# Kernel optimization log

Hardware: AMD Instinct MI355X
Metric: run time of the kernel (lower is better)

Reference implementation:

```python
import jax, jax.numpy as jnp
import numpy as np

B, S, HID = 2, 2048, 1024
H, D = 16, 64  # num query heads, head_dim; single shared KV head
SCALE = D ** -0.5


def setup_inputs() -> dict:
    key = jax.random.key(0)
    k1, k2, k3, k4, k5 = jax.random.split(key, 5)
    return {
        "hidden_states": jax.random.normal(k1, (B, S, HID), dtype=jnp.float32),
        "Wq": jax.random.normal(k2, (HID, HID), dtype=jnp.float32) * 0.02,
        "Wk": jax.random.normal(k3, (HID, D), dtype=jnp.float32) * 0.02,
        "Wv": jax.random.normal(k4, (HID, D), dtype=jnp.float32) * 0.02,
        "Wo": jax.random.normal(k5, (HID, HID), dtype=jnp.float32) * 0.02,
    }


def reference(hidden_states, Wq, Wk, Wv, Wo):
    b, s, _ = hidden_states.shape
    # projections: Q has H heads; K/V have a single shared head of dim D
    q = (hidden_states @ Wq).reshape(b, s, H, D)  # [B,S,H,D]
    k = hidden_states @ Wk                        # [B,S,D]
    v = hidden_states @ Wv                        # [B,S,D]
    # scores: broadcast single KV head across all query heads
    scores = jnp.einsum("bqhd,bkd->bhqk", q, k) * SCALE  # [B,H,S,S]
    attn = jax.nn.softmax(scores, axis=-1)
    out = jnp.einsum("bhqk,bkd->bqhd", attn, v).reshape(b, s, HID)
    return out @ Wo
```

## Files before the change

### kernel.cpp

```cpp
#include <hip/hip_runtime.h>
#include <math.h>

#define BATCH 2
#define SEQ   2048
#define HID   1024
#define NH    16
#define HD    64
#define MTOT  (BATCH * SEQ)

#define PST 72
#define VST 136
#define WTS 69

#define EXP_C1 0.1803368801111255f

typedef __attribute__((ext_vector_type(8))) short short8;
typedef __attribute__((ext_vector_type(4))) float floatx4;
typedef __attribute__((ext_vector_type(16))) float floatx16;
typedef __attribute__((ext_vector_type(4))) unsigned int uint4v;

#define MFMA32(a, b, c) __builtin_amdgcn_mfma_f32_32x32x16_bf16(a, b, c, 0, 0, 0)
#define MFMA16(a, b, c) __builtin_amdgcn_mfma_f32_16x16x32_bf16(a, b, c, 0, 0, 0)

static __device__ __forceinline__ floatx16 zero16() {
    floatx16 z;
    #pragma unroll
    for (int i = 0; i < 16; ++i) z[i] = 0.f;
    return z;
}

__device__ __forceinline__ unsigned short f2bf(float x) {
    unsigned u = __float_as_uint(x);
    u += 0x7FFF + ((u >> 16) & 1);
    return (unsigned short)(u >> 16);
}
__device__ __forceinline__ float bf2f(unsigned short h) {
    return __uint_as_float((unsigned)h << 16);
}
__device__ __forceinline__ void split16(const float* f, unsigned short* hh, unsigned short* ll) {
    #pragma unroll
    for (int e = 0; e < 16; ++e) {
        unsigned short h = f2bf(f[e]);
        hh[e] = h;
        ll[e] = f2bf(f[e] - bf2f(h));
    }
}

__device__ __forceinline__ void gld16(const unsigned short* g, unsigned short* l) {
    __builtin_amdgcn_global_load_lds(
        (const __attribute__((address_space(1))) unsigned int*)g,
        (__attribute__((address_space(3))) unsigned int*)l, 16, 0, 0);
}


__global__ __launch_bounds__(256)
void presplit_kernel(const float* __restrict__ Wq, const float* __restrict__ Wk,
                     const float* __restrict__ Wv, const float* __restrict__ Wo,
                     const float* __restrict__ X,
                     unsigned short* __restrict__ WqTh, unsigned short* __restrict__ WqTl,
                     unsigned short* __restrict__ WkTh, unsigned short* __restrict__ WkTl,
                     unsigned short* __restrict__ WvTh, unsigned short* __restrict__ WvTl,
                     unsigned short* __restrict__ WoTh, unsigned short* __restrict__ WoTl,
                     unsigned short* __restrict__ Xh)
{
    __shared__ __align__(16) float Wtmp[64][WTS];
    const int tid = threadIdx.x;
    int bx = blockIdx.x;

    if (bx >= 544) {
        size_t i0 = (size_t)(bx - 544) * 4096 + tid * 16;
        float f[16];
        *(float4*)&f[0]  = *(const float4*)(X + i0 + 0);
        *(float4*)&f[4]  = *(const float4*)(X + i0 + 4);
        *(float4*)&f[8]  = *(const float4*)(X + i0 + 8);
        *(float4*)&f[12] = *(const float4*)(X + i0 + 12);
        unsigned short hh[16];
        #pragma unroll
        for (int e = 0; e < 16; ++e) hh[e] = f2bf(f[e]);
        const int m  = (bx - 544) * 4 + (tid >> 6);
        const int k0 = (tid & 63) * 16;
        const int m32 = m >> 5, mi = (m >> 4) & 1, tr = m & 15;
        #pragma unroll
        for (int c = 0; c < 2; ++c) {
            const int k = k0 + c * 8;
            const int ktx = k >> 6, ksx = (k >> 5) & 1, qd = (k >> 3) & 3;
            size_t off = (((size_t)(m32 * 16 + ktx) * 2 + ksx) * 2 + mi) * 512
                       + (qd * 16 + tr) * 8;
            *(uint4*)(Xh + off) = *(uint4*)&hh[c * 8];
        }
        return;
    }

    const float* W; unsigned short *Th, *Tl; int ldw, kt, nt;
    if (bx < 256)      { W = Wq; Th = WqTh; Tl = WqTl; ldw = HID; kt = bx >> 4; nt = bx & 15; }
    else if (bx < 272) { W = Wk; Th = WkTh; Tl = WkTl; ldw = HD;  kt = bx - 256; nt = 0; }
    else if (bx < 288) { W = Wv; Th = WvTh; Tl = WvTl; ldw = HD;  kt = bx - 272; nt = 0; }
    else               { W = Wo; Th = WoTh; Tl = WoTl; ldw = HID; bx -= 288; kt = bx >> 4; nt = bx & 15; }
    const int k0 = kt * 64, n0 = nt * 64;

    {
        const int wk = tid >> 2, wn = (tid & 3) * 16;
        const float* wp = W + (size_t)(k0 + wk) * ldw + n0 + wn;
        float f[16];
        *(float4*)&f[0]  = *(const float4*)(wp + 0);
        *(float4*)&f[4]  = *(const float4*)(wp + 4);
        *(float4*)&f[8]  = *(const float4*)(wp + 8);
        *(float4*)&f[12] = *(const float4*)(wp + 12);
        #pragma unroll
        for (int e = 0; e < 16; ++e) Wtmp[wk][wn + e] = f[e];
    }
    __syncthreads();
    {
        const int rn = tid >> 2, rk = (tid & 3) * 16;
        float f[16];
        #pragma unroll
        for (int e = 0; e < 16; ++e) f[e] = Wtmp[rk + e][rn];
        unsigned short hh[16], ll[16];
        split16(f, hh, ll);
        const int sub = rn >> 4, tw = rn & 15;
        const size_t tb = ((size_t)nt * 16 + kt) * 4096;
        const int ksA = rk >> 5,       qA = (rk >> 3) & 3;
        const int ksB = (rk + 8) >> 5, qB = ((rk + 8) >> 3) & 3;
        const size_t offA = tb + (size_t)(ksA * 4 + sub) * 512 + (qA * 16 + tw) * 8;
        const size_t offB = tb + (size_t)(ksB * 4 + sub) * 512 + (qB * 16 + tw) * 8;
        *(uint4*)(Th + offA) = *(uint4*)&hh[0];
        *(uint4*)(Th + offB) = *(uint4*)&hh[8];
        *(uint4*)(Tl + offA) = *(uint4*)&ll[0];
        *(uint4*)(Tl + offB) = *(uint4*)&ll[8];
    }
}

__global__ __launch_bounds__(256)
void qkv_kernel(const unsigned short* __restrict__ Xfo,
                const unsigned short* __restrict__ WqTh, const unsigned short* __restrict__ WqTl,
                const unsigned short* __restrict__ WkTh, const unsigned short* __restrict__ WkTl,
                const unsigned short* __restrict__ WvTh, const unsigned short* __restrict__ WvTl,
                unsigned short* __restrict__ Qh,
                unsigned short* __restrict__ Kh, unsigned short* __restrict__ Vth)
{
    __shared__ __align__(16) unsigned short Wst[2][2][4096];

    const int tid  = threadIdx.x;
    const int wave = tid >> 6, lane = tid & 63;
    const int t = lane & 15, quad = lane >> 4;
    const int m0 = blockIdx.x * 128;
    const int nb = blockIdx.y;

    const unsigned short *WTh, *WTl; int nt;
    if (nb < 16)       { WTh = WqTh; WTl = WqTl; nt = nb; }
    else if (nb == 16) { WTh = WkTh; WTl = WkTl; nt = 0; }
    else               { WTh = WvTh; WTl = WvTl; nt = 0; }

    floatx4 acc[2][4];
    #pragma unroll
    for (int mi = 0; mi < 2; ++mi)
        #pragma unroll
        for (int sub = 0; sub < 4; ++sub) acc[mi][sub] = (floatx4){0.f,0.f,0.f,0.f};

    const size_t abase = ((size_t)(blockIdx.x * 4 + wave) * 16) * 2048 + lane * 8;
    const int g0 = wave * 2;

    auto STAGE = [&](int buf, int kt) {
        const size_t tb = ((size_t)nt * 16 + kt) * 4096 + g0 * 512 + lane * 8;
        gld16(WTh + tb,       &Wst[buf][0][g0 * 512]);
        gld16(WTh + tb + 512, &Wst[buf][0][g0 * 512 + 512]);
        gld16(WTl + tb,       &Wst[buf][1][g0 * 512]);
        gld16(WTl + tb + 512, &Wst[buf][1][g0 * 512 + 512]);
    };
    auto COMPUTE = [&](int buf, short8 a00, short8 a01, short8 a10, short8 a11) {
        #pragma unroll
        for (int ksq = 0; ksq < 2; ++ksq) {
            short8 am0 = ksq ? a10 : a00;
            short8 am1 = ksq ? a11 : a01;
            #pragma unroll
            for (int sub = 0; sub < 4; ++sub) {
                const int g = ksq * 4 + sub;
                short8 bh = *(const short8*)&Wst[buf][0][g * 512 + lane * 8];
                short8 bl = *(const short8*)&Wst[buf][1][g * 512 + lane * 8];
                acc[0][sub] = MFMA16(am0, bh, acc[0][sub]);
                acc[0][sub] = MFMA16(am0, bl, acc[0][sub]);
                acc[1][sub] = MFMA16(am1, bh, acc[1][sub]);
                acc[1][sub] = MFMA16(am1, bl, acc[1][sub]);
            }
        }
    };

    short8 a00, a01, a10, a11;
    {
        const unsigned short* ab = Xfo + abase;
        a00 = *(const short8*)(ab);
        a01 = *(const short8*)(ab + 512);
        a10 = *(const short8*)(ab + 1024);
        a11 = *(const short8*)(ab + 1536);
    }
    STAGE(0, 0);
    __syncthreads();

    int cur = 0;
    for (int kt = 0; kt < HID / 64 - 1; ++kt) {
        STAGE(cur ^ 1, kt + 1);
        const unsigned short* ab = Xfo + abase + (size_t)(kt + 1) * 2048;
        short8 n00 = *(const short8*)(ab);
        short8 n01 = *(const short8*)(ab + 512);
        short8 n10 = *(const short8*)(ab + 1024);
        short8 n11 = *(const short8*)(ab + 1536);

        COMPUTE(cur, a00, a01, a10, a11);

        __syncthreads();
        a00 = n00; a01 = n01; a10 = n10; a11 = n11;
        cur ^= 1;
    }
    COMPUTE(cur, a00, a01, a10, a11);

    #pragma unroll
    for (int mi = 0; mi < 2; ++mi)
        #pragma unroll
        for (int sub = 0; sub < 4; ++sub)
            #pragma unroll
            for (int r = 0; r < 4; ++r) {
                int g = m0 + wave * 32 + mi * 16 + quad * 4 + r;
                int d = sub * 16 + t;
                if (nb < 16) {
                    int b = g >> 11, s = g & (SEQ - 1);
                    Qh[((size_t)(b * NH + nb) * SEQ + s) * HD + d] =
                        f2bf(acc[mi][sub][r] * EXP_C1);
                } else if (nb == 16) {
                    Kh[(size_t)g * HD + d] = f2bf(acc[mi][sub][r]);
                } else {
                    int b = g >> 11, s = g & (SEQ - 1);
                    Vth[(size_t)b * HD * SEQ + (size_t)d * SEQ + s] = f2bf(acc[mi][sub][r]);
                }
            }
}

__global__ __launch_bounds__(512, 4)
void flash_kernel(const unsigned short* __restrict__ Qhg,
                  const unsigned short* __restrict__ Khg,
                  const unsigned short* __restrict__ Vthg,
                  unsigned short* __restrict__ Oh)
{
    __shared__ __align__(16) char smem[35840];
    unsigned short (*Ksh)[PST] = (unsigned short (*)[PST])smem;
    unsigned short (*Vsh)[VST] = (unsigned short (*)[VST])(smem + 18432);

    const int tid  = threadIdx.x;
    const int wave = tid >> 6, lane = tid & 63;
    const int lq = lane & 31, hi = lane >> 5;
    const int qw = wave >> 1;
    const int ks = wave & 1;
    const int klq = (lq & ~12) | ((lq & 4) << 1) | ((lq & 8) >> 1);

    const int q0 = blockIdx.x * 128;
    const int h  = blockIdx.y;
    const int b  = blockIdx.z;

    short8 qreg[4];
    {
        const unsigned short* qp =
            Qhg + ((size_t)(b * NH + h) * SEQ + q0 + qw * 32 + lq) * HD + hi * 8;
        #pragma unroll
        for (int dc = 0; dc < 4; ++dc) qreg[dc] = *(const short8*)(qp + dc * 16);
    }

    const unsigned short* Kh_b  = Khg  + (size_t)b * SEQ * HD;
    const unsigned short* Vth_b = Vthg + (size_t)b * HD * SEQ;

    const int krA = tid >> 3,          kcA = (tid & 7) * 8;
    const int krB = 64 + (tid >> 3),   kcB = kcA;
    const int vrA = tid >> 4,          vcA = (tid & 15) * 8;
    const int vrB = 32 + (tid >> 4),   vcB = vcA;

    floatx16 o0 = zero16(), o1 = zero16(), ol = zero16();
    short8 onesB;
    #pragma unroll
    for (int j = 0; j < 8; ++j) onesB[j] = (short)0x3F80;

    uint4 gk0 = *(const uint4*)(Kh_b + (size_t)krA * HD + kcA);
    uint4 gk1 = *(const uint4*)(Kh_b + (size_t)krB * HD + kcB);
    uint4 gv0 = *(const uint4*)(Vth_b + (size_t)vrA * SEQ + vcA);
    uint4 gv1 = *(const uint4*)(Vth_b + (size_t)vrB * SEQ + vcB);

    for (int kt = 0; kt < SEQ / 128; ++kt) {
        __syncthreads();
        *(uint4*)&Ksh[krA][kcA] = gk0;
        *(uint4*)&Ksh[krB][kcB] = gk1;
        *(uint4*)&Vsh[vrA][vcA] = gv0;
        *(uint4*)&Vsh[vrB][vcB] = gv1;
        if (kt + 1 < SEQ / 128) {
            gk0 = *(const uint4*)(Kh_b + (size_t)((kt + 1) * 128 + krA) * HD + kcA);
            gk1 = *(const uint4*)(Kh_b + (size_t)((kt + 1) * 128 + krB) * HD + kcB);
            gv0 = *(const uint4*)(Vth_b + (size_t)vrA * SEQ + (kt + 1) * 128 + vcA);
            gv1 = *(const uint4*)(Vth_b + (size_t)vrB * SEQ + (kt + 1) * 128 + vcB);
        }
        __syncthreads();

        #pragma unroll
        for (int c = 0; c < 2; ++c) {
            const int kb = ks * 64 + c * 32;

            floatx16 sf = zero16();
            __builtin_amdgcn_s_setprio(1);
            #pragma unroll
            for (int dc = 0; dc < 4; ++dc) {
                short8 kf = *(const short8*)&Ksh[kb + klq][dc * 16 + hi * 8];
                sf = MFMA32(kf, qreg[dc], sf);
            }
            __builtin_amdgcn_s_setprio(0);

            #pragma unroll
            for (int mm = 0; mm < 2; ++mm) {
                unsigned uu[8];
                #pragma unroll
                for (int j = 0; j < 8; ++j)
                    uu[j] = __float_as_uint(exp2f(sf[mm * 8 + j]));
                uint4v pw;
                pw.x = (uu[0] >> 16) | (uu[1] & 0xFFFF0000u);
                pw.y = (uu[2] >> 16) | (uu[3] & 0xFFFF0000u);
                pw.z = (uu[4] >> 16) | (uu[5] & 0xFFFF0000u);
                pw.w = (uu[6] >> 16) | (uu[7] & 0xFFFF0000u);
                short8 pa = __builtin_bit_cast(short8, pw);
                short8 v0 = *(const short8*)&Vsh[lq][kb + mm * 16 + hi * 8];
                short8 v1 = *(const short8*)&Vsh[32 + lq][kb + mm * 16 + hi * 8];
                __builtin_amdgcn_s_setprio(1);
                ol = MFMA32(pa, onesB, ol);
                o0 = MFMA32(pa, v0, o0);
                o1 = MFMA32(pa, v1, o1);
                __builtin_amdgcn_s_setprio(0);
            }
        }
    }

    __syncthreads();
    float* cb  = (float*)smem;
    float* cbl = (float*)(smem + 33792);
    const int cbase = (qw * 64 + lane) * 33;
    if (ks) {
        #pragma unroll
        for (int r = 0; r < 16; ++r) { cb[cbase + r] = o0[r]; cb[cbase + 16 + r] = o1[r]; }
        if (lq == 0) {
            #pragma unroll
            for (int r = 0; r < 16; ++r) cbl[(qw * 2 + hi) * 16 + r] = ol[r];
        }
    }
    __syncthreads();
    if (!ks) {
        const int m32 = b * 64 + blockIdx.x * 4 + qw;
        #pragma unroll
        for (int r = 0; r < 16; ++r) {
            int qr = (r & 3) + 8 * (r >> 2) + 4 * hi;
            float ltot = ol[r] + cbl[(qw * 2 + hi) * 16 + r];
            float inv = 1.0f / ltot;
            float a0 = o0[r] + cb[cbase + r];
            float a1 = o1[r] + cb[cbase + 16 + r];
            int mi = qr >> 4, tr = qr & 15;
            size_t base = (((size_t)(m32 * 16 + h) * 2 + 0) * 2 + mi) * 512
                        + ((lq >> 3) * 16 + tr) * 8 + (lq & 7);
            Oh[base]        = f2bf(a0 * inv);
            Oh[base + 1024] = f2bf(a1 * inv);
        }
    }
}

__global__ __launch_bounds__(256)
void out_proj_kernel(const unsigned short* __restrict__ Ofo,
                     const unsigned short* __restrict__ WoTh,
                     const unsigned short* __restrict__ WoTl,
                     float* __restrict__ out)
{
    __shared__ __align__(16) unsigned short Wst[2][2][4096];

    const int tid  = threadIdx.x;
    const int wave = tid >> 6, lane = tid & 63;
    const int t = lane & 15, quad = lane >> 4;
    const int m0 = blockIdx.x * 128;
    const int nt = blockIdx.y;

    floatx4 acc[2][4];
    #pragma unroll
    for (int mi = 0; mi < 2; ++mi)
        #pragma unroll
        for (int sub = 0; sub < 4; ++sub) acc[mi][sub] = (floatx4){0.f,0.f,0.f,0.f};

    const size_t abase = ((size_t)(blockIdx.x * 4 + wave) * 16) * 2048 + lane * 8;
    const int g0 = wave * 2;

    auto STAGE = [&](int buf, int kt) {
        const size_t tb = ((size_t)nt * 16 + kt) * 4096 + g0 * 512 + lane * 8;
        gld16(WoTh + tb,       &Wst[buf][0][g0 * 512]);
        gld16(WoTh + tb + 512, &Wst[buf][0][g0 * 512 + 512]);
        gld16(WoTl + tb,       &Wst[buf][1][g0 * 512]);
        gld16(WoTl + tb + 512, &Wst[buf][1][g0 * 512 + 512]);
    };
    auto COMPUTE = [&](int buf, short8 a00, short8 a01, short8 a10, short8 a11) {
        #pragma unroll
        for (int ksq = 0; ksq < 2; ++ksq) {
            short8 am0 = ksq ? a10 : a00;
            short8 am1 = ksq ? a11 : a01;
            #pragma unroll
            for (int sub = 0; sub < 4; ++sub) {
                const int g = ksq * 4 + sub;
                short8 bh = *(const short8*)&Wst[buf][0][g * 512 + lane * 8];
                short8 bl = *(const short8*)&Wst[buf][1][g * 512 + lane * 8];
                acc[0][sub] = MFMA16(am0, bh, acc[0][sub]);
                acc[0][sub] = MFMA16(am0, bl, acc[0][sub]);
                acc[1][sub] = MFMA16(am1, bh, acc[1][sub]);
                acc[1][sub] = MFMA16(am1, bl, acc[1][sub]);
            }
        }
    };

    short8 a00, a01, a10, a11;
    {
        const unsigned short* ab = Ofo + abase;
        a00 = *(const short8*)(ab);
        a01 = *(const short8*)(ab + 512);
        a10 = *(const short8*)(ab + 1024);
        a11 = *(const short8*)(ab + 1536);
    }
    STAGE(0, 0);
    __syncthreads();

    int cur = 0;
    for (int kt = 0; kt < HID / 64 - 1; ++kt) {
        STAGE(cur ^ 1, kt + 1);
        const unsigned short* ab = Ofo + abase + (size_t)(kt + 1) * 2048;
        short8 n00 = *(const short8*)(ab);
        short8 n01 = *(const short8*)(ab + 512);
        short8 n10 = *(const short8*)(ab + 1024);
        short8 n11 = *(const short8*)(ab + 1536);

        COMPUTE(cur, a00, a01, a10, a11);

        __syncthreads();
        a00 = n00; a01 = n01; a10 = n10; a11 = n11;
        cur ^= 1;
    }
    COMPUTE(cur, a00, a01, a10, a11);

    const int n0 = nt * 64;
    #pragma unroll
    for (int mi = 0; mi < 2; ++mi)
        #pragma unroll
        for (int sub = 0; sub < 4; ++sub)
            #pragma unroll
            for (int r = 0; r < 4; ++r)
                out[(size_t)(m0 + wave * 32 + mi * 16 + quad * 4 + r) * HID
                    + n0 + sub * 16 + t] = acc[mi][sub][r];
}

extern "C" void kernel_launch(void* const* d_in, const int* in_sizes, int n_in,
                              void* d_out, int out_size, void* d_ws, size_t ws_size,
                              hipStream_t stream)
{
    const float* X  = (const float*)d_in[0];
    const float* Wq = (const float*)d_in[1];
    const float* Wk = (const float*)d_in[2];
    const float* Wv = (const float*)d_in[3];
    const float* Wo = (const float*)d_in[4];
    float* out = (float*)d_out;

    unsigned short* Qh = (unsigned short*)d_out;
    unsigned short* Xh = Qh + (size_t)BATCH * NH * SEQ * HD;

    char* ws = (char*)d_ws;
    const size_t SZ_WQ = (size_t)HID * HID * 2;
    const size_t SZ_WK = (size_t)HD * HID * 2;
    unsigned short* WqTh = (unsigned short*)(ws);
    unsigned short* WqTl = (unsigned short*)(ws + SZ_WQ);
    unsigned short* WkTh = (unsigned short*)(ws + 2*SZ_WQ);
    unsigned short* WkTl = (unsigned short*)(ws + 2*SZ_WQ + SZ_WK);
    unsigned short* WvTh = (unsigned short*)(ws + 2*SZ_WQ + 2*SZ_WK);
    unsigned short* WvTl = (unsigned short*)(ws + 2*SZ_WQ + 3*SZ_WK);
    unsigned short* WoTh = (unsigned short*)(ws + 2*SZ_WQ + 4*SZ_WK);
    unsigned short* WoTl = (unsigned short*)(ws + 3*SZ_WQ + 4*SZ_WK);
    unsigned short* Kh   = (unsigned short*)(ws + 4*SZ_WQ + 4*SZ_WK);
    unsigned short* Vth  = (unsigned short*)(ws + 4*SZ_WQ + 4*SZ_WK + (size_t)MTOT*HD*2);
    unsigned short* Oh   = (unsigned short*)(ws + 4*SZ_WQ + 4*SZ_WK + (size_t)MTOT*HD*4);

    presplit_kernel<<<dim3(1568), 256, 0, stream>>>(Wq, Wk, Wv, Wo, X,
        WqTh, WqTl, WkTh, WkTl, WvTh, WvTl, WoTh, WoTl, Xh);
    qkv_kernel<<<dim3(MTOT / 128, 18), 256, 0, stream>>>(Xh,
        WqTh, WqTl, WkTh, WkTl, WvTh, WvTl, Qh, Kh, Vth);
    flash_kernel<<<dim3(SEQ / 128, NH, BATCH), 512, 0, stream>>>(Qh, Kh, Vth, Oh);
    out_proj_kernel<<<dim3(MTOT / 128, HID / 64), 256, 0, stream>>>(Oh, WoTh, WoTl, out);
}
```

Baseline: 174.4 us.

## Drop low-half weight split in QKV projection and widen GEMM blocks to 512 threads

```diff
diff --git a/kernel.cpp b/kernel.cpp
--- a/kernel.cpp
+++ b/kernel.cpp
@@ -37,14 +37,6 @@
 __device__ __forceinline__ float bf2f(unsigned short h) {
     return __uint_as_float((unsigned)h << 16);
 }
-__device__ __forceinline__ void split16(const float* f, unsigned short* hh, unsigned short* ll) {
-    #pragma unroll
-    for (int e = 0; e < 16; ++e) {
-        unsigned short h = f2bf(f[e]);
-        hh[e] = h;
-        ll[e] = f2bf(f[e] - bf2f(h));
-    }
-}
 
 __device__ __forceinline__ void gld16(const unsigned short* g, unsigned short* l) {
     __builtin_amdgcn_global_load_lds(
@@ -57,9 +49,9 @@
 void presplit_kernel(const float* __restrict__ Wq, const float* __restrict__ Wk,
                      const float* __restrict__ Wv, const float* __restrict__ Wo,
                      const float* __restrict__ X,
-                     unsigned short* __restrict__ WqTh, unsigned short* __restrict__ WqTl,
-                     unsigned short* __restrict__ WkTh, unsigned short* __restrict__ WkTl,
-                     unsigned short* __restrict__ WvTh, unsigned short* __restrict__ WvTl,
+                     unsigned short* __restrict__ WqTh,
+                     unsigned short* __restrict__ WkTh,
+                     unsigned short* __restrict__ WvTh,
                      unsigned short* __restrict__ WoTh, unsigned short* __restrict__ WoTl,
                      unsigned short* __restrict__ Xh)
 {
@@ -92,10 +84,10 @@
     }
 
     const float* W; unsigned short *Th, *Tl; int ldw, kt, nt;
-    if (bx < 256)      { W = Wq; Th = WqTh; Tl = WqTl; ldw = HID; kt = bx >> 4; nt = bx & 15; }
-    else if (bx < 272) { W = Wk; Th = WkTh; Tl = WkTl; ldw = HD;  kt = bx - 256; nt = 0; }
-    else if (bx < 288) { W = Wv; Th = WvTh; Tl = WvTl; ldw = HD;  kt = bx - 272; nt = 0; }
-    else               { W = Wo; Th = WoTh; Tl = WoTl; ldw = HID; bx -= 288; kt = bx >> 4; nt = bx & 15; }
+    if (bx < 256)      { W = Wq; Th = WqTh; Tl = nullptr; ldw = HID; kt = bx >> 4; nt = bx & 15; }
+    else if (bx < 272) { W = Wk; Th = WkTh; Tl = nullptr; ldw = HD;  kt = bx - 256; nt = 0; }
+    else if (bx < 288) { W = Wv; Th = WvTh; Tl = nullptr; ldw = HD;  kt = bx - 272; nt = 0; }
+    else               { W = Wo; Th = WoTh; Tl = WoTl;   ldw = HID; bx -= 288; kt = bx >> 4; nt = bx & 15; }
     const int k0 = kt * 64, n0 = nt * 64;
 
     {
@@ -115,8 +107,9 @@
         float f[16];
         #pragma unroll
         for (int e = 0; e < 16; ++e) f[e] = Wtmp[rk + e][rn];
-        unsigned short hh[16], ll[16];
-        split16(f, hh, ll);
+        unsigned short hh[16];
+        #pragma unroll
+        for (int e = 0; e < 16; ++e) hh[e] = f2bf(f[e]);
         const int sub = rn >> 4, tw = rn & 15;
         const size_t tb = ((size_t)nt * 16 + kt) * 4096;
         const int ksA = rk >> 5,       qA = (rk >> 3) & 3;
@@ -125,20 +118,25 @@
         const size_t offB = tb + (size_t)(ksB * 4 + sub) * 512 + (qB * 16 + tw) * 8;
         *(uint4*)(Th + offA) = *(uint4*)&hh[0];
         *(uint4*)(Th + offB) = *(uint4*)&hh[8];
-        *(uint4*)(Tl + offA) = *(uint4*)&ll[0];
-        *(uint4*)(Tl + offB) = *(uint4*)&ll[8];
-    }
-}
-
-__global__ __launch_bounds__(256)
+        if (Tl) {
+            unsigned short ll[16];
+            #pragma unroll
+            for (int e = 0; e < 16; ++e) ll[e] = f2bf(f[e] - bf2f(hh[e]));
+            *(uint4*)(Tl + offA) = *(uint4*)&ll[0];
+            *(uint4*)(Tl + offB) = *(uint4*)&ll[8];
+        }
+    }
+}
+
+__global__ __launch_bounds__(512)
 void qkv_kernel(const unsigned short* __restrict__ Xfo,
-                const unsigned short* __restrict__ WqTh, const unsigned short* __restrict__ WqTl,
-                const unsigned short* __restrict__ WkTh, const unsigned short* __restrict__ WkTl,
-                const unsigned short* __restrict__ WvTh, const unsigned short* __restrict__ WvTl,
+                const unsigned short* __restrict__ WqTh,
+                const unsigned short* __restrict__ WkTh,
+                const unsigned short* __restrict__ WvTh,
                 unsigned short* __restrict__ Qh,
                 unsigned short* __restrict__ Kh, unsigned short* __restrict__ Vth)
 {
-    __shared__ __align__(16) unsigned short Wst[2][2][4096];
+    __shared__ __align__(16) unsigned short Wst[2][4096];
 
     const int tid  = threadIdx.x;
     const int wave = tid >> 6, lane = tid & 63;
@@ -146,92 +144,70 @@
     const int m0 = blockIdx.x * 128;
     const int nb = blockIdx.y;
 
-    const unsigned short *WTh, *WTl; int nt;
-    if (nb < 16)       { WTh = WqTh; WTl = WqTl; nt = nb; }
-    else if (nb == 16) { WTh = WkTh; WTl = WkTl; nt = 0; }
-    else               { WTh = WvTh; WTl = WvTl; nt = 0; }
-
-    floatx4 acc[2][4];
-    #pragma unroll
-    for (int mi = 0; mi < 2; ++mi)
-        #pragma unroll
-        for (int sub = 0; sub < 4; ++sub) acc[mi][sub] = (floatx4){0.f,0.f,0.f,0.f};
-
-    const size_t abase = ((size_t)(blockIdx.x * 4 + wave) * 16) * 2048 + lane * 8;
-    const int g0 = wave * 2;
+    const unsigned short *WTh; int nt;
+    if (nb < 16)       { WTh = WqTh; nt = nb; }
+    else if (nb == 16) { WTh = WkTh; nt = 0; }
+    else               { WTh = WvTh; nt = 0; }
+
+    floatx4 acc[4];
+    #pragma unroll
+    for (int sub = 0; sub < 4; ++sub) acc[sub] = (floatx4){0.f,0.f,0.f,0.f};
+
+    const int m32 = blockIdx.x * 4 + (wave >> 1), mi = wave & 1;
+    const size_t abase = ((size_t)m32 * 16) * 2048 + (size_t)mi * 512 + lane * 8;
 
     auto STAGE = [&](int buf, int kt) {
-        const size_t tb = ((size_t)nt * 16 + kt) * 4096 + g0 * 512 + lane * 8;
-        gld16(WTh + tb,       &Wst[buf][0][g0 * 512]);
-        gld16(WTh + tb + 512, &Wst[buf][0][g0 * 512 + 512]);
-        gld16(WTl + tb,       &Wst[buf][1][g0 * 512]);
-        gld16(WTl + tb + 512, &Wst[buf][1][g0 * 512 + 512]);
+        const size_t tb = ((size_t)nt * 16 + kt) * 4096 + wave * 512 + lane * 8;
+        gld16(WTh + tb, &Wst[buf][wave * 512]);
     };
-    auto COMPUTE = [&](int buf, short8 a00, short8 a01, short8 a10, short8 a11) {
+    auto COMPUTE = [&](int buf, short8 a0, short8 a1) {
         #pragma unroll
         for (int ksq = 0; ksq < 2; ++ksq) {
-            short8 am0 = ksq ? a10 : a00;
-            short8 am1 = ksq ? a11 : a01;
+            short8 am = ksq ? a1 : a0;
             #pragma unroll
             for (int sub = 0; sub < 4; ++sub) {
-                const int g = ksq * 4 + sub;
-                short8 bh = *(const short8*)&Wst[buf][0][g * 512 + lane * 8];
-                short8 bl = *(const short8*)&Wst[buf][1][g * 512 + lane * 8];
-                acc[0][sub] = MFMA16(am0, bh, acc[0][sub]);
-                acc[0][sub] = MFMA16(am0, bl, acc[0][sub]);
-                acc[1][sub] = MFMA16(am1, bh, acc[1][sub]);
-                acc[1][sub] = MFMA16(am1, bl, acc[1][sub]);
+                short8 bh = *(const short8*)&Wst[buf][(ksq * 4 + sub) * 512 + lane * 8];
+                acc[sub] = MFMA16(am, bh, acc[sub]);
             }
         }
     };
 
-    short8 a00, a01, a10, a11;
-    {
-        const unsigned short* ab = Xfo + abase;
-        a00 = *(const short8*)(ab);
-        a01 = *(const short8*)(ab + 512);
-        a10 = *(const short8*)(ab + 1024);
-        a11 = *(const short8*)(ab + 1536);
-    }
+    short8 a0 = *(const short8*)(Xfo + abase);
+    short8 a1 = *(const short8*)(Xfo + abase + 1024);
     STAGE(0, 0);
     __syncthreads();
 
     int cur = 0;
     for (int kt = 0; kt < HID / 64 - 1; ++kt) {
         STAGE(cur ^ 1, kt + 1);
-        const unsigned short* ab = Xfo + abase + (size_t)(kt + 1) * 2048;
-        short8 n00 = *(const short8*)(ab);
-        short8 n01 = *(const short8*)(ab + 512);
-        short8 n10 = *(const short8*)(ab + 1024);
-        short8 n11 = *(const short8*)(ab + 1536);
-
-        COMPUTE(cur, a00, a01, a10, a11);
+        short8 n0 = *(const short8*)(Xfo + abase + (size_t)(kt + 1) * 2048);
+        short8 n1 = *(const short8*)(Xfo + abase + (size_t)(kt + 1) * 2048 + 1024);
+
+        COMPUTE(cur, a0, a1);
 
         __syncthreads();
-        a00 = n00; a01 = n01; a10 = n10; a11 = n11;
+        a0 = n0; a1 = n1;
         cur ^= 1;
     }
-    COMPUTE(cur, a00, a01, a10, a11);
-
-    #pragma unroll
-    for (int mi = 0; mi < 2; ++mi)
-        #pragma unroll
-        for (int sub = 0; sub < 4; ++sub)
-            #pragma unroll
-            for (int r = 0; r < 4; ++r) {
-                int g = m0 + wave * 32 + mi * 16 + quad * 4 + r;
-                int d = sub * 16 + t;
-                if (nb < 16) {
-                    int b = g >> 11, s = g & (SEQ - 1);
-                    Qh[((size_t)(b * NH + nb) * SEQ + s) * HD + d] =
-                        f2bf(acc[mi][sub][r] * EXP_C1);
-                } else if (nb == 16) {
-                    Kh[(size_t)g * HD + d] = f2bf(acc[mi][sub][r]);
-                } else {
-                    int b = g >> 11, s = g & (SEQ - 1);
-                    Vth[(size_t)b * HD * SEQ + (size_t)d * SEQ + s] = f2bf(acc[mi][sub][r]);
-                }
+    COMPUTE(cur, a0, a1);
+
+    #pragma unroll
+    for (int sub = 0; sub < 4; ++sub)
+        #pragma unroll
+        for (int r = 0; r < 4; ++r) {
+            int g = m0 + wave * 16 + quad * 4 + r;
+            int d = sub * 16 + t;
+            if (nb < 16) {
+                int b = g >> 11, s = g & (SEQ - 1);
+                Qh[((size_t)(b * NH + nb) * SEQ + s) * HD + d] =
+                    f2bf(acc[sub][r] * EXP_C1);
+            } else if (nb == 16) {
+                Kh[(size_t)g * HD + d] = f2bf(acc[sub][r]);
+            } else {
+                int b = g >> 11, s = g & (SEQ - 1);
+                Vth[(size_t)b * HD * SEQ + (size_t)d * SEQ + s] = f2bf(acc[sub][r]);
             }
+        }
 }
 
 __global__ __launch_bounds__(512, 4)
@@ -362,7 +338,7 @@
     }
 }
 
-__global__ __launch_bounds__(256)
+__global__ __launch_bounds__(512)
 void out_proj_kernel(const unsigned short* __restrict__ Ofo,
                      const unsigned short* __restrict__ WoTh,
                      const unsigned short* __restrict__ WoTl,
@@ -376,77 +352,58 @@
     const int m0 = blockIdx.x * 128;
     const int nt = blockIdx.y;
 
-    floatx4 acc[2][4];
-    #pragma unroll
-    for (int mi = 0; mi < 2; ++mi)
-        #pragma unroll
-        for (int sub = 0; sub < 4; ++sub) acc[mi][sub] = (floatx4){0.f,0.f,0.f,0.f};
-
-    const size_t abase = ((size_t)(blockIdx.x * 4 + wave) * 16) * 2048 + lane * 8;
-    const int g0 = wave * 2;
+    floatx4 acc[4];
+    #pragma unroll
+    for (int sub = 0; sub < 4; ++sub) acc[sub] = (floatx4){0.f,0.f,0.f,0.f};
+
+    const int m32 = blockIdx.x * 4 + (wave >> 1), mi = wave & 1;
+    const size_t abase = ((size_t)m32 * 16) * 2048 + (size_t)mi * 512 + lane * 8;
 
     auto STAGE = [&](int buf, int kt) {
-        const size_t tb = ((size_t)nt * 16 + kt) * 4096 + g0 * 512 + lane * 8;
-        gld16(WoTh + tb,       &Wst[buf][0][g0 * 512]);
-        gld16(WoTh + tb + 512, &Wst[buf][0][g0 * 512 + 512]);
-        gld16(WoTl + tb,       &Wst[buf][1][g0 * 512]);
-        gld16(WoTl + tb + 512, &Wst[buf][1][g0 * 512 + 512]);
+        const size_t tb = ((size_t)nt * 16 + kt) * 4096 + wave * 512 + lane * 8;
+        gld16(WoTh + tb, &Wst[buf][0][wave * 512]);
+        gld16(WoTl + tb, &Wst[buf][1][wave * 512]);
     };
-    auto COMPUTE = [&](int buf, short8 a00, short8 a01, short8 a10, short8 a11) {
+    auto COMPUTE = [&](int buf, short8 a0, short8 a1) {
         #pragma unroll
         for (int ksq = 0; ksq < 2; ++ksq) {
-            short8 am0 = ksq ? a10 : a00;
-            short8 am1 = ksq ? a11 : a01;
+            short8 am = ksq ? a1 : a0;
             #pragma unroll
             for (int sub = 0; sub < 4; ++sub) {
-                const int g = ksq * 4 + sub;
-                short8 bh = *(const short8*)&Wst[buf][0][g * 512 + lane * 8];
-                short8 bl = *(const short8*)&Wst[buf][1][g * 512 + lane * 8];
-                acc[0][sub] = MFMA16(am0, bh, acc[0][sub]);
-                acc[0][sub] = MFMA16(am0, bl, acc[0][sub]);
-                acc[1][sub] = MFMA16(am1, bh, acc[1][sub]);
-                acc[1][sub] = MFMA16(am1, bl, acc[1][sub]);
+                short8 bh = *(const short8*)&Wst[buf][0][(ksq * 4 + sub) * 512 + lane * 8];
+                short8 bl = *(const short8*)&Wst[buf][1][(ksq * 4 + sub) * 512 + lane * 8];
+                acc[sub] = MFMA16(am, bh, acc[sub]);
+                acc[sub] = MFMA16(am, bl, acc[sub]);
             }
         }
     };
 
-    short8 a00, a01, a10, a11;
-    {
-        const unsigned short* ab = Ofo + abase;
-        a00 = *(const short8*)(ab);
-        a01 = *(const short8*)(ab + 512);
-        a10 = *(const short8*)(ab + 1024);
-        a11 = *(const short8*)(ab + 1536);
-    }
+    short8 a0 = *(const short8*)(Ofo + abase);
+    short8 a1 = *(const short8*)(Ofo + abase + 1024);
     STAGE(0, 0);
     __syncthreads();
 
     int cur = 0;
     for (int kt = 0; kt < HID / 64 - 1; ++kt) {
         STAGE(cur ^ 1, kt + 1);
-        const unsigned short* ab = Ofo + abase + (size_t)(kt + 1) * 2048;
-        short8 n00 = *(const short8*)(ab);
-        short8 n01 = *(const short8*)(ab + 512);
-        short8 n10 = *(const short8*)(ab + 1024);
-        short8 n11 = *(const short8*)(ab + 1536);
-
-        COMPUTE(cur, a00, a01, a10, a11);
+        short8 n0 = *(const short8*)(Ofo + abase + (size_t)(kt + 1) * 2048);
+        short8 n1 = *(const short8*)(Ofo + abase + (size_t)(kt + 1) * 2048 + 1024);
+
+        COMPUTE(cur, a0, a1);
 
         __syncthreads();
-        a00 = n00; a01 = n01; a10 = n10; a11 = n11;
+        a0 = n0; a1 = n1;
         cur ^= 1;
     }
-    COMPUTE(cur, a00, a01, a10, a11);
+    COMPUTE(cur, a0, a1);
 
     const int n0 = nt * 64;
     #pragma unroll
-    for (int mi = 0; mi < 2; ++mi)
-        #pragma unroll
-        for (int sub = 0; sub < 4; ++sub)
-            #pragma unroll
-            for (int r = 0; r < 4; ++r)
-                out[(size_t)(m0 + wave * 32 + mi * 16 + quad * 4 + r) * HID
-                    + n0 + sub * 16 + t] = acc[mi][sub][r];
+    for (int sub = 0; sub < 4; ++sub)
+        #pragma unroll
+        for (int r = 0; r < 4; ++r)
+            out[(size_t)(m0 + wave * 16 + quad * 4 + r) * HID
+                + n0 + sub * 16 + t] = acc[sub][r];
 }
 
 extern "C" void kernel_launch(void* const* d_in, const int* in_sizes, int n_in,
@@ -467,11 +424,8 @@
     const size_t SZ_WQ = (size_t)HID * HID * 2;
     const size_t SZ_WK = (size_t)HD * HID * 2;
     unsigned short* WqTh = (unsigned short*)(ws);
-    unsigned short* WqTl = (unsigned short*)(ws + SZ_WQ);
     unsigned short* WkTh = (unsigned short*)(ws + 2*SZ_WQ);
-    unsigned short* WkTl = (unsigned short*)(ws + 2*SZ_WQ + SZ_WK);
     unsigned short* WvTh = (unsigned short*)(ws + 2*SZ_WQ + 2*SZ_WK);
-    unsigned short* WvTl = (unsigned short*)(ws + 2*SZ_WQ + 3*SZ_WK);
     unsigned short* WoTh = (unsigned short*)(ws + 2*SZ_WQ + 4*SZ_WK);
     unsigned short* WoTl = (unsigned short*)(ws + 3*SZ_WQ + 4*SZ_WK);
     unsigned short* Kh   = (unsigned short*)(ws + 4*SZ_WQ + 4*SZ_WK);
@@ -479,9 +433,9 @@
     unsigned short* Oh   = (unsigned short*)(ws + 4*SZ_WQ + 4*SZ_WK + (size_t)MTOT*HD*4);
 
     presplit_kernel<<<dim3(1568), 256, 0, stream>>>(Wq, Wk, Wv, Wo, X,
-        WqTh, WqTl, WkTh, WkTl, WvTh, WvTl, WoTh, WoTl, Xh);
-    qkv_kernel<<<dim3(MTOT / 128, 18), 256, 0, stream>>>(Xh,
-        WqTh, WqTl, WkTh, WkTl, WvTh, WvTl, Qh, Kh, Vth);
+        WqTh, WkTh, WvTh, WoTh, WoTl, Xh);
+    qkv_kernel<<<dim3(MTOT / 128, 18), 512, 0, stream>>>(Xh,
+        WqTh, WkTh, WvTh, Qh, Kh, Vth);
     flash_kernel<<<dim3(SEQ / 128, NH, BATCH), 512, 0, stream>>>(Qh, Kh, Vth, Oh);
-    out_proj_kernel<<<dim3(MTOT / 128, HID / 64), 256, 0, stream>>>(Oh, WoTh, WoTl, out);
-}
+    out_proj_kernel<<<dim3(MTOT / 128, HID / 64), 512, 0, stream>>>(Oh, WoTh, WoTl, out);
+}
```

New measurement: 174.4 us. No clear change (+0.0%).
